# Kernel optimization log

Hardware: AMD Instinct MI355X
Metric: run time of the kernel (lower is better)

The kernel has to match this reference:

```python
import jax, jax.numpy as jnp
import numpy as np

B, T, D = 16384, 4, 1024
H = 16
HD = D // H
R = 8
ALPHA = 16
SCALING = ALPHA / R  # 2.0
SCALE = HD ** -0.5


def setup_inputs() -> dict:
    key = jax.random.key(0)
    ks = jax.random.split(key, 10)
    inp = {
        "x": jax.random.normal(ks[0], (B, T, D), jnp.float32),
        "temporal_pos": jax.random.normal(ks[1], (1, T, D), jnp.float32) * 0.02,
        # store linear weights as [in, out] so y = x @ W (math-equivalent to torch's x @ W.T)
        "W_qkv": jax.random.normal(ks[2], (D, 3 * D), jnp.float32) * (D ** -0.5),
        "lora_q_A": jax.random.normal(ks[3], (D, R), jnp.float32) * 0.01,
        "lora_q_B": jax.random.normal(ks[4], (R, D), jnp.float32) * 0.01,  # nonzero so grads flow
        "lora_v_A": jax.random.normal(ks[5], (D, R), jnp.float32) * 0.01,
        "lora_v_B": jax.random.normal(ks[6], (R, D), jnp.float32) * 0.01,
        "W_proj": jax.random.normal(ks[7], (D, D), jnp.float32) * (D ** -0.5),
        "b_proj": jax.random.normal(ks[8], (D,), jnp.float32) * 0.01,
        "lora_proj_A": jax.random.normal(ks[9], (D, R), jnp.float32) * 0.01,
        "lora_proj_B": jax.random.normal(jax.random.fold_in(key, 99), (R, D), jnp.float32) * 0.01,
    }
    return inp


def reference(x, temporal_pos, W_qkv, lora_q_A, lora_q_B, lora_v_A, lora_v_B,
              W_proj, b_proj, lora_proj_A, lora_proj_B):
    b, t, d = x.shape
    x = x + temporal_pos[:, :t, :]                       # [B,T,D]
    qkv = (x @ W_qkv).reshape(b, t, 3, H, HD)
    qkv = jnp.transpose(qkv, (2, 0, 3, 1, 4))            # [3,B,H,T,hd]
    q, k, v = qkv[0], qkv[1], qkv[2]
    dq = ((x @ lora_q_A) @ lora_q_B).reshape(b, t, H, HD)
    dq = jnp.transpose(dq, (0, 2, 1, 3)) * SCALING
    dv = ((x @ lora_v_A) @ lora_v_B).reshape(b, t, H, HD)
    dv = jnp.transpose(dv, (0, 2, 1, 3)) * SCALING
    q = q + dq
    v = v + dv
    attn = jax.nn.softmax(jnp.einsum('bhqd,bhkd->bhqk', q, k) * SCALE, axis=-1)
    # dropout is identity in eval mode
    out = jnp.einsum('bhqk,bhkd->bhqd', attn, v)         # [B,H,T,hd]
    out = jnp.transpose(out, (0, 2, 1, 3)).reshape(b, t, d)
    out = (out @ W_proj + b_proj) + ((out @ lora_proj_A) @ lora_proj_B) * SCALING
    return out.mean(axis=1)                              # [B,D]
```

## Files before the change

kernel.cpp:

```cpp
#include <hip/hip_runtime.h>

typedef unsigned short u16;
typedef unsigned int u32;
typedef short bf16x8 __attribute__((ext_vector_type(8)));
typedef float f32x4 __attribute__((ext_vector_type(4)));

__device__ __forceinline__ u16 f2bf(float f) {
    u32 u = __float_as_uint(f);
    u32 r = (u + 0x7fffu + ((u >> 16) & 1u)) >> 16;
    return (u16)r;
}
__device__ __forceinline__ float bf2f(u16 v) { return __uint_as_float(((u32)v) << 16); }
__device__ __forceinline__ float bflo(u32 u) { return __uint_as_float(u << 16); }
__device__ __forceinline__ float bfhi(u32 u) { return __uint_as_float(u & 0xffff0000u); }

__device__ __forceinline__ void load_lds16(const void* g, void* l) {
    __builtin_amdgcn_global_load_lds(
        (const __attribute__((address_space(1))) void*)(unsigned long long)g,
        (__attribute__((address_space(3))) void*)(u32)(unsigned long long)l,
        16, 0, 0);
}

__global__ __launch_bounds__(256) void k_w(
    const float* __restrict__ Wqkv,
    const float* __restrict__ Aq, const float* __restrict__ Bq,
    const float* __restrict__ Av, const float* __restrict__ Bv,
    const float* __restrict__ Wp, const float* __restrict__ Ap,
    const float* __restrict__ Bp,
    u16* __restrict__ WqkvT, u16* __restrict__ WprojT)
{
    int e = blockIdx.x * 256 + threadIdx.x;
    if (e < 3145728) {
        int k = e / 3072;
        int n = e - k * 3072;
        float w = Wqkv[e];
        if (n < 1024) {
            float d = 0.f;
#pragma unroll
            for (int r = 0; r < 8; ++r) d += Aq[k * 8 + r] * Bq[r * 1024 + n];
            w += 2.f * d;
        } else if (n >= 2048) {
            int n2 = n - 2048;
            float d = 0.f;
#pragma unroll
            for (int r = 0; r < 8; ++r) d += Av[k * 8 + r] * Bv[r * 1024 + n2];
            w += 2.f * d;
        }
        WqkvT[(size_t)n * 1024 + k] = f2bf(w);
    } else {
        int e2 = e - 3145728;
        int k = e2 >> 10, n = e2 & 1023;
        float d = 0.f;
#pragma unroll
        for (int r = 0; r < 8; ++r) d += Ap[k * 8 + r] * Bp[r * 1024 + n];
        WprojT[(size_t)n * 1024 + k] = f2bf(Wp[e2] + 2.f * d);
    }
}

__global__ __launch_bounds__(256) void k0_prep(
    const float* __restrict__ x, const float* __restrict__ tpos,
    u16* __restrict__ xb)
{
    size_t idx = ((size_t)blockIdx.x * 256 + threadIdx.x) * 8;
    int col = (int)(idx & 1023);
    int t = (int)((idx >> 10) & 3);
    const float4* xp = (const float4*)(x + idx);
    const float4* tp = (const float4*)(tpos + t * 1024 + col);
    float4 a0 = xp[0], a1 = xp[1];
    float4 b0 = tp[0], b1 = tp[1];
    u32 p0 = (u32)f2bf(a0.x + b0.x) | ((u32)f2bf(a0.y + b0.y) << 16);
    u32 p1 = (u32)f2bf(a0.z + b0.z) | ((u32)f2bf(a0.w + b0.w) << 16);
    u32 p2 = (u32)f2bf(a1.x + b1.x) | ((u32)f2bf(a1.y + b1.y) << 16);
    u32 p3 = (u32)f2bf(a1.z + b1.z) | ((u32)f2bf(a1.w + b1.w) << 16);
    *(uint4*)(xb + idx) = make_uint4(p0, p1, p2, p3);
}

__global__ __launch_bounds__(256) void k1_qkv_attn(
    const u16* __restrict__ xb, const u16* __restrict__ WqkvT,
    u16* __restrict__ obar)
{
    __shared__ __align__(16) char smem[53760];
    u16* stage = (u16*)smem;
    u16* qkv = (u16*)smem;
    float* S = (float*)(smem + 51200);
    float* wP = (float*)(smem + 53248);

    const int tid = threadIdx.x;
    const int lane = tid & 63;
    const int wid = tid >> 6;
    const int wm = wid & 1;
    const int wn = wid >> 1;
    const int lm = lane & 15;
    const int lk = lane >> 4;
    const int h = blockIdx.x;
    const int mt = blockIdx.y;

    u32 goff[10];
#pragma unroll
    for (int i = 0; i < 10; ++i) {
        int c = i * 256 + tid;
        if (i < 4) {
            int row = c >> 3, cc = c & 7;
            int cc2 = cc ^ (row & 7);
            goff[i] = (u32)((mt * 128 + row) * 1024 + cc2 * 8);
        } else {
            int cb = c - 1024;
            int n = cb >> 3, cc = cb & 7;
            int cc2 = cc ^ (n & 7);
            int strip = n >> 6, j = n & 63;
            goff[i] = (u32)(((strip << 10) + h * 64 + j) * 1024 + cc2 * 8);
        }
    }

    f32x4 acc[4][6];
#pragma unroll
    for (int a = 0; a < 4; ++a)
#pragma unroll
        for (int b = 0; b < 6; ++b) acc[a][b] = (f32x4){0.f, 0.f, 0.f, 0.f};

    for (int kt = 0; kt < 16; ++kt) {
        const int k0 = kt * 64;
        __syncthreads();
#pragma unroll
        for (int i = 0; i < 10; ++i) {
            const u16* g = (i < 4 ? xb : WqkvT) + goff[i] + k0;
            load_lds16((const void*)g, (void*)(smem + i * 4096 + tid * 16));
        }
        __syncthreads();
#pragma unroll
        for (int kk = 0; kk < 2; ++kk) {
            const int kb = kk * 4 + lk;
            bf16x8 af[4], bfr[6];
#pragma unroll
            for (int im = 0; im < 4; ++im) {
                int m = wm * 64 + im * 16 + lm;
                af[im] = *(const bf16x8*)(stage + (m * 8 + (kb ^ (m & 7))) * 8);
            }
#pragma unroll
            for (int in = 0; in < 6; ++in) {
                int n = wn * 96 + in * 16 + lm;
                bfr[in] = *(const bf16x8*)(stage + 8192 + (n * 8 + (kb ^ (n & 7))) * 8);
            }
#pragma unroll
            for (int im = 0; im < 4; ++im)
#pragma unroll
                for (int in = 0; in < 6; ++in)
                    acc[im][in] = __builtin_amdgcn_mfma_f32_16x16x32_bf16(
                        af[im], bfr[in], acc[im][in], 0, 0, 0);
        }
    }

    __syncthreads();
#pragma unroll
    for (int im = 0; im < 4; ++im) {
#pragma unroll
        for (int in = 0; in < 6; ++in) {
            int col = wn * 96 + in * 16 + lm;
            int rowb = wm * 64 + im * 16 + lk * 4;
#pragma unroll
            for (int r = 0; r < 4; ++r)
                qkv[(rowb + r) * 200 + col] = f2bf(acc[im][in][r]);
        }
    }
    __syncthreads();

#pragma unroll
    for (int it = 0; it < 2; ++it) {
        int task = tid + it * 256;
        int bl = task >> 4, t = (task >> 2) & 3, u = task & 3;
        const u32* q4 = (const u32*)(qkv + (bl * 4 + t) * 200);
        const u32* k4 = (const u32*)(qkv + (bl * 4 + u) * 200 + 64);
        float s = 0.f;
#pragma unroll
        for (int d = 0; d < 32; ++d) {
            u32 qa = q4[d], ka = k4[d];
            s += bflo(qa) * bflo(ka) + bfhi(qa) * bfhi(ka);
        }
        S[bl * 16 + t * 4 + u] = s * 0.125f;
    }
    __syncthreads();
    if (tid < 128) {
        float* sp = S + (tid >> 2) * 16 + (tid & 3) * 4;
        float s0 = sp[0], s1 = sp[1], s2 = sp[2], s3 = sp[3];
        float mx = fmaxf(fmaxf(s0, s1), fmaxf(s2, s3));
        float e0 = __expf(s0 - mx), e1 = __expf(s1 - mx);
        float e2 = __expf(s2 - mx), e3 = __expf(s3 - mx);
        float inv = 0.25f / (e0 + e1 + e2 + e3);
        sp[0] = e0 * inv; sp[1] = e1 * inv; sp[2] = e2 * inv; sp[3] = e3 * inv;
    }
    __syncthreads();
    if (tid < 128) {
        int bl = tid >> 2, u = tid & 3;
        wP[bl * 4 + u] = S[bl * 16 + u] + S[bl * 16 + 4 + u] +
                         S[bl * 16 + 8 + u] + S[bl * 16 + 12 + u];
    }
    __syncthreads();
    {
        int bl = tid >> 3, db = (tid & 7) * 8;
        float w0 = wP[bl * 4 + 0], w1 = wP[bl * 4 + 1];
        float w2 = wP[bl * 4 + 2], w3 = wP[bl * 4 + 3];
        const u16* v0 = qkv + (bl * 4 + 0) * 200 + 128 + db;
        const u16* v1 = v0 + 200;
        const u16* v2 = v1 + 200;
        const u16* v3 = v2 + 200;
        u16 ov[8];
#pragma unroll
        for (int j = 0; j < 8; ++j) {
            float val = w0 * bf2f(v0[j]) + w1 * bf2f(v1[j]) +
                        w2 * bf2f(v2[j]) + w3 * bf2f(v3[j]);
            ov[j] = f2bf(val);
        }
        u32 p0 = (u32)ov[0] | ((u32)ov[1] << 16);
        u32 p1 = (u32)ov[2] | ((u32)ov[3] << 16);
        u32 p2 = (u32)ov[4] | ((u32)ov[5] << 16);
        u32 p3 = (u32)ov[6] | ((u32)ov[7] << 16);
        size_t brow = (size_t)mt * 32 + bl;
        *(uint4*)(obar + brow * 1024 + h * 64 + db) = make_uint4(p0, p1, p2, p3);
    }
}

__global__ __launch_bounds__(256) void k2_proj(
    const u16* __restrict__ obar, const u16* __restrict__ WprojT,
    const float* __restrict__ bias, float* __restrict__ out)
{
    __shared__ __align__(16) char smem[32768];
    u16* stage = (u16*)smem;
    const int tid = threadIdx.x;
    const int lane = tid & 63;
    const int wid = tid >> 6;
    const int wm = wid & 1, wn = wid >> 1;
    const int lm = lane & 15, lk = lane >> 4;
    const int nt = blockIdx.x;
    const int mt = blockIdx.y;

    u32 goff[8];
#pragma unroll
    for (int i = 0; i < 8; ++i) {
        int c = i * 256 + tid;
        if (i < 4) {
            int row = c >> 3, cc2 = (c & 7) ^ (row & 7);
            goff[i] = (u32)((mt * 128 + row) * 1024 + cc2 * 8);
        } else {
            int cb = c - 1024;
            int n = cb >> 3, cc2 = (cb & 7) ^ (n & 7);
            goff[i] = (u32)((nt * 128 + n) * 1024 + cc2 * 8);
        }
    }

    f32x4 acc[4][4];
#pragma unroll
    for (int a = 0; a < 4; ++a)
#pragma unroll
        for (int b = 0; b < 4; ++b) acc[a][b] = (f32x4){0.f, 0.f, 0.f, 0.f};

    for (int kt = 0; kt < 16; ++kt) {
        const int k0 = kt * 64;
        __syncthreads();
#pragma unroll
        for (int i = 0; i < 8; ++i) {
            const u16* g = (i < 4 ? obar : WprojT) + goff[i] + k0;
            load_lds16((const void*)g, (void*)(smem + i * 4096 + tid * 16));
        }
        __syncthreads();
#pragma unroll
        for (int kk = 0; kk < 2; ++kk) {
            const int kb = kk * 4 + lk;
            bf16x8 af[4], bfr[4];
#pragma unroll
            for (int im = 0; im < 4; ++im) {
                int m = wm * 64 + im * 16 + lm;
                af[im] = *(const bf16x8*)(stage + (m * 8 + (kb ^ (m & 7))) * 8);
            }
#pragma unroll
            for (int in = 0; in < 4; ++in) {
                int n = wn * 64 + in * 16 + lm;
                bfr[in] = *(const bf16x8*)(stage + 8192 + (n * 8 + (kb ^ (n & 7))) * 8);
            }
#pragma unroll
            for (int im = 0; im < 4; ++im)
#pragma unroll
                for (int in = 0; in < 4; ++in)
                    acc[im][in] = __builtin_amdgcn_mfma_f32_16x16x32_bf16(
                        af[im], bfr[in], acc[im][in], 0, 0, 0);
        }
    }

    float bv[4];
#pragma unroll
    for (int in = 0; in < 4; ++in) bv[in] = bias[nt * 128 + wn * 64 + in * 16 + lm];
#pragma unroll
    for (int im = 0; im < 4; ++im)
#pragma unroll
        for (int in = 0; in < 4; ++in) {
            int col = nt * 128 + wn * 64 + in * 16 + lm;
#pragma unroll
            for (int r = 0; r < 4; ++r) {
                int row = mt * 128 + wm * 64 + im * 16 + lk * 4 + r;
                out[(size_t)row * 1024 + col] = acc[im][in][r] + bv[in];
            }
        }
}

extern "C" void kernel_launch(void* const* d_in, const int* in_sizes, int n_in,
                              void* d_out, int out_size, void* d_ws, size_t ws_size,
                              hipStream_t stream)
{
    const float* x     = (const float*)d_in[0];
    const float* tpos  = (const float*)d_in[1];
    const float* Wqkv  = (const float*)d_in[2];
    const float* Aq    = (const float*)d_in[3];
    const float* Bq    = (const float*)d_in[4];
    const float* Av    = (const float*)d_in[5];
    const float* Bv    = (const float*)d_in[6];
    const float* Wp    = (const float*)d_in[7];
    const float* bp    = (const float*)d_in[8];
    const float* Ap    = (const float*)d_in[9];
    const float* Bp    = (const float*)d_in[10];
    float* out = (float*)d_out;

    char* ws = (char*)d_ws;
    u16* xb     = (u16*)ws;
    u16* obar   = (u16*)(ws + 134217728);
    u16* WqkvT  = (u16*)(ws + 134217728 + 33554432);
    u16* WprojT = (u16*)(ws + 134217728 + 33554432 + 6291456);

    hipLaunchKernelGGL(k_w, dim3(16384), dim3(256), 0, stream,
                       Wqkv, Aq, Bq, Av, Bv, Wp, Ap, Bp, WqkvT, WprojT);
    hipLaunchKernelGGL(k0_prep, dim3(32768), dim3(256), 0, stream, x, tpos, xb);
    hipLaunchKernelGGL(k1_qkv_attn, dim3(16, 512), dim3(256), 0, stream,
                       xb, WqkvT, obar);
    hipLaunchKernelGGL(k2_proj, dim3(8, 128), dim3(256), 0, stream,
                       obar, WprojT, bp, out);
}
```

Measured before the change: 936.1 us.

## Tile weight-prep transpose through LDS and use 512-thread QKV attention blocks

The weight-merge kernel now handles 64x64 tiles. It stages the LoRA factors and a padded transpose buffer in shared memory, so global reads and bf16 writes are coalesced instead of scattered by the transpose. The QKV+attention kernel moves from 256 to 512 threads with 8 waves (4x2). Each wave now computes a 32x96 accumulator tile, and the qkv LDS row stride shrinks from 200 to 194. The aim is lower register pressure, more resident waves, and a cheaper weight transpose, at the cost of more barrier participants and possibly more LDS bank conflicts from the odd stride.

```diff
diff --git a/kernel.cpp b/kernel.cpp
--- a/kernel.cpp
+++ b/kernel.cpp
@@ -29,31 +29,76 @@
     const float* __restrict__ Bp,
     u16* __restrict__ WqkvT, u16* __restrict__ WprojT)
 {
-    int e = blockIdx.x * 256 + threadIdx.x;
-    if (e < 3145728) {
-        int k = e / 3072;
-        int n = e - k * 3072;
-        float w = Wqkv[e];
-        if (n < 1024) {
-            float d = 0.f;
-#pragma unroll
-            for (int r = 0; r < 8; ++r) d += Aq[k * 8 + r] * Bq[r * 1024 + n];
-            w += 2.f * d;
-        } else if (n >= 2048) {
-            int n2 = n - 2048;
-            float d = 0.f;
-#pragma unroll
-            for (int r = 0; r < 8; ++r) d += Av[k * 8 + r] * Bv[r * 1024 + n2];
-            w += 2.f * d;
-        }
-        WqkvT[(size_t)n * 1024 + k] = f2bf(w);
+    __shared__ float As[512];
+    __shared__ float Bs[512];
+    __shared__ float T[64 * 65];
+
+    const int tid = threadIdx.x;
+    const int b = blockIdx.x;
+
+    const float* W; const float* Ax = nullptr; const float* Bx = nullptr;
+    u16* Wout; int ldw, k0, n0, nB = 0;
+    bool has_lora;
+    if (b < 768) {
+        int kt = b / 48, ntile = b - kt * 48;
+        k0 = kt * 64; n0 = ntile * 64;
+        W = Wqkv; ldw = 3072; Wout = WqkvT;
+        if (n0 < 1024)       { has_lora = true;  Ax = Aq; Bx = Bq; nB = n0; }
+        else if (n0 >= 2048) { has_lora = true;  Ax = Av; Bx = Bv; nB = n0 - 2048; }
+        else                 { has_lora = false; }
     } else {
-        int e2 = e - 3145728;
-        int k = e2 >> 10, n = e2 & 1023;
-        float d = 0.f;
-#pragma unroll
-        for (int r = 0; r < 8; ++r) d += Ap[k * 8 + r] * Bp[r * 1024 + n];
-        WprojT[(size_t)n * 1024 + k] = f2bf(Wp[e2] + 2.f * d);
+        int b2 = b - 768;
+        int kt = b2 >> 4, ntile = b2 & 15;
+        k0 = kt * 64; n0 = ntile * 64;
+        W = Wp; ldw = 1024; Wout = WprojT;
+        has_lora = true; Ax = Ap; Bx = Bp; nB = n0;
+    }
+
+    if (has_lora) {
+#pragma unroll
+        for (int it = 0; it < 2; ++it) {
+            int idx = tid + it * 256;
+            As[idx] = Ax[(k0 + (idx >> 3)) * 8 + (idx & 7)];
+            Bs[idx] = Bx[(idx >> 6) * 1024 + nB + (idx & 63)];
+        }
+    }
+    __syncthreads();
+
+    const int r8 = tid >> 3;
+    const int c = tid & 7;
+#pragma unroll
+    for (int it = 0; it < 2; ++it) {
+        int kl = r8 + it * 32;
+        const float* wrow = W + (size_t)(k0 + kl) * ldw + n0 + c * 8;
+        float4 w0 = *(const float4*)wrow;
+        float4 w1 = *(const float4*)(wrow + 4);
+        float wv[8] = {w0.x, w0.y, w0.z, w0.w, w1.x, w1.y, w1.z, w1.w};
+        if (has_lora) {
+#pragma unroll
+            for (int j = 0; j < 8; ++j) {
+                float d = 0.f;
+#pragma unroll
+                for (int r = 0; r < 8; ++r) d += As[kl * 8 + r] * Bs[r * 64 + c * 8 + j];
+                wv[j] += 2.f * d;
+            }
+        }
+#pragma unroll
+        for (int j = 0; j < 8; ++j) T[(c * 8 + j) * 65 + kl] = wv[j];
+    }
+    __syncthreads();
+
+#pragma unroll
+    for (int it = 0; it < 2; ++it) {
+        int nl = r8 + it * 32;
+        u16 o[8];
+#pragma unroll
+        for (int j = 0; j < 8; ++j) o[j] = f2bf(T[nl * 65 + c * 8 + j]);
+        u32 p0 = (u32)o[0] | ((u32)o[1] << 16);
+        u32 p1 = (u32)o[2] | ((u32)o[3] << 16);
+        u32 p2 = (u32)o[4] | ((u32)o[5] << 16);
+        u32 p3 = (u32)o[6] | ((u32)o[7] << 16);
+        *(uint4*)(Wout + (size_t)(n0 + nl) * 1024 + k0 + c * 8) =
+            make_uint4(p0, p1, p2, p3);
     }
 }
 
@@ -75,65 +120,63 @@
     *(uint4*)(xb + idx) = make_uint4(p0, p1, p2, p3);
 }
 
-__global__ __launch_bounds__(256) void k1_qkv_attn(
+__global__ __launch_bounds__(512, 4) void k1_qkv_attn(
     const u16* __restrict__ xb, const u16* __restrict__ WqkvT,
     u16* __restrict__ obar)
 {
-    __shared__ __align__(16) char smem[53760];
+    __shared__ __align__(16) char smem[52224];
     u16* stage = (u16*)smem;
     u16* qkv = (u16*)smem;
-    float* S = (float*)(smem + 51200);
-    float* wP = (float*)(smem + 53248);
+    float* S = (float*)(smem + 49664);
+    float* wP = (float*)(smem + 51712);
 
     const int tid = threadIdx.x;
     const int lane = tid & 63;
     const int wid = tid >> 6;
-    const int wm = wid & 1;
-    const int wn = wid >> 1;
+    const int wm = wid & 3;
+    const int wn = wid >> 2;
     const int lm = lane & 15;
     const int lk = lane >> 4;
     const int h = blockIdx.x;
     const int mt = blockIdx.y;
 
-    u32 goff[10];
-#pragma unroll
-    for (int i = 0; i < 10; ++i) {
-        int c = i * 256 + tid;
-        if (i < 4) {
-            int row = c >> 3, cc = c & 7;
-            int cc2 = cc ^ (row & 7);
+    u32 goff[5];
+#pragma unroll
+    for (int i = 0; i < 5; ++i) {
+        int c = i * 512 + tid;
+        if (c < 1024) {
+            int row = c >> 3, cc2 = (c & 7) ^ (row & 7);
             goff[i] = (u32)((mt * 128 + row) * 1024 + cc2 * 8);
         } else {
             int cb = c - 1024;
-            int n = cb >> 3, cc = cb & 7;
-            int cc2 = cc ^ (n & 7);
+            int n = cb >> 3, cc2 = (cb & 7) ^ (n & 7);
             int strip = n >> 6, j = n & 63;
             goff[i] = (u32)(((strip << 10) + h * 64 + j) * 1024 + cc2 * 8);
         }
     }
 
-    f32x4 acc[4][6];
-#pragma unroll
-    for (int a = 0; a < 4; ++a)
-#pragma unroll
-        for (int b = 0; b < 6; ++b) acc[a][b] = (f32x4){0.f, 0.f, 0.f, 0.f};
+    f32x4 acc[2][6];
+#pragma unroll
+    for (int a = 0; a < 2; ++a)
+#pragma unroll
+        for (int bb = 0; bb < 6; ++bb) acc[a][bb] = (f32x4){0.f, 0.f, 0.f, 0.f};
 
     for (int kt = 0; kt < 16; ++kt) {
         const int k0 = kt * 64;
         __syncthreads();
 #pragma unroll
-        for (int i = 0; i < 10; ++i) {
-            const u16* g = (i < 4 ? xb : WqkvT) + goff[i] + k0;
-            load_lds16((const void*)g, (void*)(smem + i * 4096 + tid * 16));
+        for (int i = 0; i < 5; ++i) {
+            const u16* g = (i < 2 ? xb : WqkvT) + goff[i] + k0;
+            load_lds16((const void*)g, (void*)(smem + i * 8192 + tid * 16));
         }
         __syncthreads();
 #pragma unroll
         for (int kk = 0; kk < 2; ++kk) {
             const int kb = kk * 4 + lk;
-            bf16x8 af[4], bfr[6];
-#pragma unroll
-            for (int im = 0; im < 4; ++im) {
-                int m = wm * 64 + im * 16 + lm;
+            bf16x8 af[2], bfr[6];
+#pragma unroll
+            for (int im = 0; im < 2; ++im) {
+                int m = wm * 32 + im * 16 + lm;
                 af[im] = *(const bf16x8*)(stage + (m * 8 + (kb ^ (m & 7))) * 8);
             }
 #pragma unroll
@@ -142,7 +185,7 @@
                 bfr[in] = *(const bf16x8*)(stage + 8192 + (n * 8 + (kb ^ (n & 7))) * 8);
             }
 #pragma unroll
-            for (int im = 0; im < 4; ++im)
+            for (int im = 0; im < 2; ++im)
 #pragma unroll
                 for (int in = 0; in < 6; ++in)
                     acc[im][in] = __builtin_amdgcn_mfma_f32_16x16x32_bf16(
@@ -152,24 +195,22 @@
 
     __syncthreads();
 #pragma unroll
-    for (int im = 0; im < 4; ++im) {
+    for (int im = 0; im < 2; ++im) {
 #pragma unroll
         for (int in = 0; in < 6; ++in) {
             int col = wn * 96 + in * 16 + lm;
-            int rowb = wm * 64 + im * 16 + lk * 4;
+            int rowb = wm * 32 + im * 16 + lk * 4;
 #pragma unroll
             for (int r = 0; r < 4; ++r)
-                qkv[(rowb + r) * 200 + col] = f2bf(acc[im][in][r]);
-        }
-    }
-    __syncthreads();
-
-#pragma unroll
-    for (int it = 0; it < 2; ++it) {
-        int task = tid + it * 256;
-        int bl = task >> 4, t = (task >> 2) & 3, u = task & 3;
-        const u32* q4 = (const u32*)(qkv + (bl * 4 + t) * 200);
-        const u32* k4 = (const u32*)(qkv + (bl * 4 + u) * 200 + 64);
+                qkv[(rowb + r) * 194 + col] = f2bf(acc[im][in][r]);
+        }
+    }
+    __syncthreads();
+
+    {
+        int bl = tid >> 4, t = (tid >> 2) & 3, u = tid & 3;
+        const u32* q4 = (const u32*)(qkv + (bl * 4 + t) * 194);
+        const u32* k4 = (const u32*)(qkv + (bl * 4 + u) * 194 + 64);
         float s = 0.f;
 #pragma unroll
         for (int d = 0; d < 32; ++d) {
@@ -195,14 +236,14 @@
                          S[bl * 16 + 8 + u] + S[bl * 16 + 12 + u];
     }
     __syncthreads();
-    {
+    if (tid < 256) {
         int bl = tid >> 3, db = (tid & 7) * 8;
         float w0 = wP[bl * 4 + 0], w1 = wP[bl * 4 + 1];
         float w2 = wP[bl * 4 + 2], w3 = wP[bl * 4 + 3];
-        const u16* v0 = qkv + (bl * 4 + 0) * 200 + 128 + db;
-        const u16* v1 = v0 + 200;
-        const u16* v2 = v1 + 200;
-        const u16* v3 = v2 + 200;
+        const u16* v0 = qkv + (bl * 4 + 0) * 194 + 128 + db;
+        const u16* v1 = v0 + 194;
+        const u16* v2 = v1 + 194;
+        const u16* v3 = v2 + 194;
         u16 ov[8];
 #pragma unroll
         for (int j = 0; j < 8; ++j) {
@@ -251,7 +292,7 @@
 #pragma unroll
     for (int a = 0; a < 4; ++a)
 #pragma unroll
-        for (int b = 0; b < 4; ++b) acc[a][b] = (f32x4){0.f, 0.f, 0.f, 0.f};
+        for (int bb = 0; bb < 4; ++bb) acc[a][bb] = (f32x4){0.f, 0.f, 0.f, 0.f};
 
     for (int kt = 0; kt < 16; ++kt) {
         const int k0 = kt * 64;
@@ -324,10 +365,10 @@
     u16* WqkvT  = (u16*)(ws + 134217728 + 33554432);
     u16* WprojT = (u16*)(ws + 134217728 + 33554432 + 6291456);
 
-    hipLaunchKernelGGL(k_w, dim3(16384), dim3(256), 0, stream,
+    hipLaunchKernelGGL(k_w, dim3(1024), dim3(256), 0, stream,
                        Wqkv, Aq, Bq, Av, Bv, Wp, Ap, Bp, WqkvT, WprojT);
     hipLaunchKernelGGL(k0_prep, dim3(32768), dim3(256), 0, stream, x, tpos, xb);
-    hipLaunchKernelGGL(k1_qkv_attn, dim3(16, 512), dim3(256), 0, stream,
+    hipLaunchKernelGGL(k1_qkv_attn, dim3(16, 512), dim3(512), 0, stream,
                        xb, WqkvT, obar);
     hipLaunchKernelGGL(k2_proj, dim3(8, 128), dim3(256), 0, stream,
                        obar, WprojT, bp, out);
```

Measured after the change: 875.1 us. 1.07x faster.
